# Kernel optimization log

Hardware: AMD Instinct MI355X
Metric: run time of the kernel (lower is better)

The kernel has to match this reference:

```python
import jax, jax.numpy as jnp
import numpy as np

N, D, C = 32768, 1024, 256
GAMMA = 1e-4


def setup_inputs() -> dict:
    key = jax.random.key(0)
    kx, kw = jax.random.split(key)
    X = jax.random.normal(kx, (N, D), dtype=jnp.float32)
    # lcls linear params: weight [C, D], bias [C] (torch nn.Linear layout)
    W = jax.random.normal(kw, (C, D), dtype=jnp.float32) * (1.0 / np.sqrt(D))
    b = jnp.zeros((C,), dtype=jnp.float32)
    return {"X": X, "W": W, "b": b}


def reference(X, W, b):
    # P = softmax(X @ W.T + b) over cluster dim C
    P = jax.nn.softmax(X @ W.T + b, axis=-1)            # [N, C]
    # Reorder P @ P.T @ X -> P @ (P.T @ X): avoids the O(N^2) affinity matrix
    PtX = jnp.einsum('nc,nd->cd', P, X)                  # [C, D]
    return X + GAMMA * (P @ PtX)                         # [N, D]
```

## Files before the change

kernel.cpp:

```cpp
#include <hip/hip_runtime.h>
#include <hip/hip_bf16.h>
#include <stdint.h>

#define N_TOK 32768
#define DIM   1024
#define NC    256
#define GAMMA_F 1e-4f

typedef unsigned short u16;
typedef __attribute__((ext_vector_type(8))) short bf16x8;
typedef __attribute__((ext_vector_type(4))) float f32x4;

__device__ __forceinline__ u16 f2b(float f) {
  union { float f; uint32_t u; } c; c.f = f;
  uint32_t u = c.u;
  return (u16)((u + 0x7FFFu + ((u >> 16) & 1u)) >> 16);
}

__device__ __forceinline__ void gll16(const void* g, void* l) {
  __builtin_amdgcn_global_load_lds(
      (const __attribute__((address_space(1))) unsigned int*)g,
      (__attribute__((address_space(3))) unsigned int*)l, 16, 0, 0);
}


__global__ __launch_bounds__(256) void k0_transpose(const float* __restrict__ X,
                                                    u16* __restrict__ TX) {
  __shared__ u16 tile[64][68];
  const int n0 = blockIdx.x * 64;
  const int d0 = blockIdx.y * 64;
  const int t = threadIdx.x;
  const int r = t >> 4;
  const int c4 = (t & 15) * 4;
#pragma unroll
  for (int i = 0; i < 4; ++i) {
    const int row = r + i * 16;
    const float4 v = *reinterpret_cast<const float4*>(&X[(size_t)(n0 + row) * DIM + d0 + c4]);
    tile[row][c4 + 0] = f2b(v.x);
    tile[row][c4 + 1] = f2b(v.y);
    tile[row][c4 + 2] = f2b(v.z);
    tile[row][c4 + 3] = f2b(v.w);
  }
  __syncthreads();
#pragma unroll
  for (int i = 0; i < 4; ++i) {
    const int drow = r + i * 16;
    ushort4 o;
    o.x = tile[c4 + 0][drow];
    o.y = tile[c4 + 1][drow];
    o.z = tile[c4 + 2][drow];
    o.w = tile[c4 + 3][drow];
    *reinterpret_cast<ushort4*>(&TX[(size_t)(d0 + drow) * N_TOK + n0 + c4]) = o;
  }
}

__global__ __launch_bounds__(256) void k0_convert_w(const float* __restrict__ W,
                                                    u16* __restrict__ Wb) {
  const int idx = (blockIdx.x * 256 + threadIdx.x) * 4;
  const float4 v = *reinterpret_cast<const float4*>(&W[idx]);
  ushort4 o;
  o.x = f2b(v.x); o.y = f2b(v.y); o.z = f2b(v.z); o.w = f2b(v.w);
  *reinterpret_cast<ushort4*>(&Wb[idx]) = o;
}

__global__ __launch_bounds__(256, 2) void p1_fused(const float* __restrict__ X,
                                                   const u16* __restrict__ Wb,
                                                   const float* __restrict__ bias,
                                                   u16* __restrict__ P,
                                                   u16* __restrict__ PT) {
  __shared__ __align__(16) char smem[66560];
  u16* As = (u16*)smem;
  u16* Bs = (u16*)(smem + 8192);
  const int t = threadIdx.x;
  const int lane = t & 63, wave = t >> 6;
  const int wm = wave & 1, wn = wave >> 1;
  const int n0 = blockIdx.x * 64;
  const int frow = lane & 15, fq = lane >> 4;
  const int au = t & 7, ar0 = t >> 3;
  const int bug = (lane & 7) ^ (lane >> 3);

  f32x4 acc[2][8] = {};
  for (int kt = 0; kt < 16; ++kt) {
    const int k0 = kt * 64;
#pragma unroll
    for (int h = 0; h < 2; ++h) {
      const int r = ar0 + h * 32;
      const size_t gb = (size_t)(n0 + r) * DIM + k0 + au * 8;
      const float4 v0 = *reinterpret_cast<const float4*>(&X[gb]);
      const float4 v1 = *reinterpret_cast<const float4*>(&X[gb + 4]);
      bf16x8 u;
      u[0] = (short)f2b(v0.x); u[1] = (short)f2b(v0.y);
      u[2] = (short)f2b(v0.z); u[3] = (short)f2b(v0.w);
      u[4] = (short)f2b(v1.x); u[5] = (short)f2b(v1.y);
      u[6] = (short)f2b(v1.z); u[7] = (short)f2b(v1.w);
      *reinterpret_cast<bf16x8*>(&As[r * 64 + ((au ^ (r & 7)) * 8)]) = u;
    }
#pragma unroll
    for (int i = 0; i < 8; ++i) {
      const int chunk = wave * 8 + i;
      const int brow = chunk * 8 + (lane >> 3);
      gll16(&Wb[(size_t)brow * DIM + k0 + bug * 8], &Bs[chunk * 512]);
    }
    __syncthreads();
#pragma unroll
    for (int ks = 0; ks < 2; ++ks) {
      bf16x8 af[2], bg[8];
#pragma unroll
      for (int m = 0; m < 2; ++m) {
        const int r = wm * 32 + m * 16 + frow;
        af[m] = *reinterpret_cast<const bf16x8*>(&As[r * 64 + (((ks * 4 + fq) ^ (r & 7)) * 8)]);
      }
#pragma unroll
      for (int n = 0; n < 8; ++n) {
        const int r = wn * 128 + n * 16 + frow;
        bg[n] = *reinterpret_cast<const bf16x8*>(&Bs[r * 64 + (((ks * 4 + fq) ^ (r & 7)) * 8)]);
      }
#pragma unroll
      for (int m = 0; m < 2; ++m)
#pragma unroll
        for (int n = 0; n < 8; ++n)
          acc[m][n] = __builtin_amdgcn_mfma_f32_16x16x32_bf16(af[m], bg[n], acc[m][n], 0, 0, 0);
    }
    __syncthreads();
  }
  float* Sf = (float*)smem;
#pragma unroll
  for (int m = 0; m < 2; ++m)
#pragma unroll
    for (int n = 0; n < 8; ++n) {
      const int row = wm * 32 + m * 16 + fq * 4;
      const int col = wn * 128 + n * 16 + frow;
#pragma unroll
      for (int j = 0; j < 4; ++j)
        Sf[(row + j) * 260 + col] = acc[m][n][j];
    }
  __syncthreads();
  u16* Su = (u16*)smem;
  const float4 bv = *reinterpret_cast<const float4*>(&bias[lane * 4]);
  const float l2e = 1.44269504088896f;
#pragma unroll
  for (int i = 0; i < 16; ++i) {
    const int row = wave * 16 + i;
    float4 v = *reinterpret_cast<const float4*>(&Sf[row * 260 + lane * 4]);
    v.x += bv.x; v.y += bv.y; v.z += bv.z; v.w += bv.w;
    float mx = fmaxf(fmaxf(v.x, v.y), fmaxf(v.z, v.w));
#pragma unroll
    for (int s = 1; s < 64; s <<= 1) mx = fmaxf(mx, __shfl_xor(mx, s, 64));
    const float e0 = exp2f((v.x - mx) * l2e), e1 = exp2f((v.y - mx) * l2e);
    const float e2 = exp2f((v.z - mx) * l2e), e3 = exp2f((v.w - mx) * l2e);
    float sm = e0 + e1 + e2 + e3;
#pragma unroll
    for (int s = 1; s < 64; s <<= 1) sm += __shfl_xor(sm, s, 64);
    const float inv = 1.0f / sm;
    ushort4 o;
    o.x = f2b(e0 * inv); o.y = f2b(e1 * inv);
    o.z = f2b(e2 * inv); o.w = f2b(e3 * inv);
    *reinterpret_cast<ushort4*>(&P[(size_t)(n0 + row) * NC + lane * 4]) = o;
    const int rb = row & 31;
    Su[row * 520 + (((lane * 4 + 0) ^ rb)) * 2] = o.x;
    Su[row * 520 + (((lane * 4 + 1) ^ rb)) * 2] = o.y;
    Su[row * 520 + (((lane * 4 + 2) ^ rb)) * 2] = o.z;
    Su[row * 520 + (((lane * 4 + 3) ^ rb)) * 2] = o.w;
  }
  __syncthreads();
#pragma unroll
  for (int it = 0; it < 16; ++it) {
    const int c = it * 16 + wave * 4 + fq;
    const int n = frow * 4;
    ushort4 o;
    o.x = Su[(n + 0) * 520 + ((c ^ ((n + 0) & 31))) * 2];
    o.y = Su[(n + 1) * 520 + ((c ^ ((n + 1) & 31))) * 2];
    o.z = Su[(n + 2) * 520 + ((c ^ ((n + 2) & 31))) * 2];
    o.w = Su[(n + 3) * 520 + ((c ^ ((n + 3) & 31))) * 2];
    *reinterpret_cast<ushort4*>(&PT[(size_t)c * N_TOK + n0 + n]) = o;
  }
}

__global__ __launch_bounds__(256, 2) void p2_gemm(const u16* __restrict__ TX,
                                                  const u16* __restrict__ PT,
                                                  float* __restrict__ part) {
  __shared__ __align__(16) char smem[67584];
  u16* As = (u16*)smem;
  u16* Bs = (u16*)(smem + 16384);
  const int t = threadIdx.x;
  const int lane = t & 63, wave = t >> 6;
  const int wm = wave & 1, wn = wave >> 1;
  const int sk = blockIdx.x;
  const int d0 = (blockIdx.y >> 1) * 128;
  const int c0 = (blockIdx.y & 1) * 128;
  const int frow = lane & 15, fq = lane >> 4;
  const int srow = lane >> 3;
  const int bug = (lane & 7) ^ (lane >> 3);
  f32x4 acc[4][4] = {};
  for (int kt = 0; kt < 16; ++kt) {
    const size_t k0 = (size_t)sk * 1024 + kt * 64;
#pragma unroll
    for (int i = 0; i < 4; ++i) {
      const int chunk = wave * 4 + i;
      const int r = chunk * 8 + srow;
      gll16(&TX[(size_t)(d0 + r) * N_TOK + k0 + bug * 8], &As[chunk * 512]);
      gll16(&PT[(size_t)(c0 + r) * N_TOK + k0 + bug * 8], &Bs[chunk * 512]);
    }
    __syncthreads();
#pragma unroll
    for (int ks = 0; ks < 2; ++ks) {
      bf16x8 af[4], bg[4];
#pragma unroll
      for (int m = 0; m < 4; ++m) {
        const int r = wm * 64 + m * 16 + frow;
        af[m] = *reinterpret_cast<const bf16x8*>(&As[r * 64 + (((ks * 4 + fq) ^ (r & 7)) * 8)]);
      }
#pragma unroll
      for (int n = 0; n < 4; ++n) {
        const int r = wn * 64 + n * 16 + frow;
        bg[n] = *reinterpret_cast<const bf16x8*>(&Bs[r * 64 + (((ks * 4 + fq) ^ (r & 7)) * 8)]);
      }
#pragma unroll
      for (int m = 0; m < 4; ++m)
#pragma unroll
        for (int n = 0; n < 4; ++n)
          acc[m][n] = __builtin_amdgcn_mfma_f32_16x16x32_bf16(af[m], bg[n], acc[m][n], 0, 0, 0);
    }
    __syncthreads();
  }
  float* Cf = (float*)smem;
#pragma unroll
  for (int m = 0; m < 4; ++m)
#pragma unroll
    for (int n = 0; n < 4; ++n) {
      const int row = wm * 64 + m * 16 + fq * 4;
      const int col = wn * 64 + n * 16 + frow;
#pragma unroll
      for (int j = 0; j < 4; ++j)
        Cf[(row + j) * 132 + col] = acc[m][n][j];
    }
  __syncthreads();
  float* pl = part + (size_t)sk * (DIM * NC);
  const int cl = (t & 31) * 4;
  const int rr = t >> 5;
#pragma unroll
  for (int p = 0; p < 16; ++p) {
    const int row = p * 8 + rr;
    const float4 v = *reinterpret_cast<const float4*>(&Cf[row * 132 + cl]);
    *reinterpret_cast<float4*>(&pl[(size_t)(d0 + row) * NC + c0 + cl]) = v;
  }
}

__global__ __launch_bounds__(256) void k2_reduce(const float* __restrict__ part,
                                                 u16* __restrict__ PtXb) {
  const int g = (blockIdx.x * 256 + threadIdx.x) * 4;
  f32x4 s = {0.f, 0.f, 0.f, 0.f};
#pragma unroll
  for (int p = 0; p < 32; ++p)
    s += *reinterpret_cast<const f32x4*>(&part[(size_t)p * (DIM * NC) + g]);
  ushort4 o;
  o.x = f2b(s[0] * GAMMA_F); o.y = f2b(s[1] * GAMMA_F);
  o.z = f2b(s[2] * GAMMA_F); o.w = f2b(s[3] * GAMMA_F);
  *reinterpret_cast<ushort4*>(&PtXb[g]) = o;
}

__global__ __launch_bounds__(256, 2) void p3_gemm(const u16* __restrict__ P,
                                                  const u16* __restrict__ PtXb,
                                                  const float* __restrict__ X,
                                                  float* __restrict__ Out) {
  __shared__ __align__(16) char smem[67584];
  u16* As = (u16*)smem;
  u16* Bs = (u16*)(smem + 16384);
  const int t = threadIdx.x;
  const int lane = t & 63, wave = t >> 6;
  const int wm = wave & 1, wn = wave >> 1;
  const int n0 = blockIdx.x * 128;
  const int d0 = blockIdx.y * 128;
  const int frow = lane & 15, fq = lane >> 4;
  const int srow = lane >> 3;
  const int bug = (lane & 7) ^ (lane >> 3);
  f32x4 acc[4][4] = {};
  for (int kt = 0; kt < 4; ++kt) {
    const int k0 = kt * 64;
#pragma unroll
    for (int i = 0; i < 4; ++i) {
      const int chunk = wave * 4 + i;
      const int r = chunk * 8 + srow;
      gll16(&P[(size_t)(n0 + r) * NC + k0 + bug * 8], &As[chunk * 512]);
      gll16(&PtXb[(size_t)(d0 + r) * NC + k0 + bug * 8], &Bs[chunk * 512]);
    }
    __syncthreads();
#pragma unroll
    for (int ks = 0; ks < 2; ++ks) {
      bf16x8 af[4], bg[4];
#pragma unroll
      for (int m = 0; m < 4; ++m) {
        const int r = wm * 64 + m * 16 + frow;
        af[m] = *reinterpret_cast<const bf16x8*>(&As[r * 64 + (((ks * 4 + fq) ^ (r & 7)) * 8)]);
      }
#pragma unroll
      for (int n = 0; n < 4; ++n) {
        const int r = wn * 64 + n * 16 + frow;
        bg[n] = *reinterpret_cast<const bf16x8*>(&Bs[r * 64 + (((ks * 4 + fq) ^ (r & 7)) * 8)]);
      }
#pragma unroll
      for (int m = 0; m < 4; ++m)
#pragma unroll
        for (int n = 0; n < 4; ++n)
          acc[m][n] = __builtin_amdgcn_mfma_f32_16x16x32_bf16(af[m], bg[n], acc[m][n], 0, 0, 0);
    }
    __syncthreads();
  }
  float* Cf = (float*)smem;
#pragma unroll
  for (int m = 0; m < 4; ++m)
#pragma unroll
    for (int n = 0; n < 4; ++n) {
      const int row = wm * 64 + m * 16 + fq * 4;
      const int col = wn * 64 + n * 16 + frow;
#pragma unroll
      for (int j = 0; j < 4; ++j)
        Cf[(row + j) * 132 + col] = acc[m][n][j];
    }
  __syncthreads();
  const int cl = (t & 31) * 4;
  const int rr = t >> 5;
#pragma unroll
  for (int p = 0; p < 16; ++p) {
    const int row = p * 8 + rr;
    float4 v = *reinterpret_cast<const float4*>(&Cf[row * 132 + cl]);
    const size_t off = (size_t)(n0 + row) * DIM + d0 + cl;
    const float4 x = *reinterpret_cast<const float4*>(&X[off]);
    v.x += x.x; v.y += x.y; v.z += x.z; v.w += x.w;
    *reinterpret_cast<float4*>(&Out[off]) = v;
  }
}

extern "C" void kernel_launch(void* const* d_in, const int* in_sizes, int n_in,
                              void* d_out, int out_size, void* d_ws, size_t ws_size,
                              hipStream_t stream) {
  const float* X = (const float*)d_in[0];
  const float* W = (const float*)d_in[1];
  const float* b = (const float*)d_in[2];
  float* Out = (float*)d_out;
  char* ws = (char*)d_ws;

  const size_t OFF_TX   = 0;
  const size_t OFF_WB   = (size_t)64 << 20;
  const size_t OFF_PTXB = OFF_WB + ((size_t)512 << 10);
  const size_t OFF_PART = (size_t)65 << 20;
  const size_t OFF_P    = (size_t)97 << 20;
  const size_t OFF_PT   = (size_t)113 << 20;
  const size_t NEED     = (size_t)129 << 20;
  if (ws_size < NEED) return;

  u16*   TX   = (u16*)(ws + OFF_TX);
  u16*   Wb   = (u16*)(ws + OFF_WB);
  u16*   PtXb = (u16*)(ws + OFF_PTXB);
  float* part = (float*)(ws + OFF_PART);
  u16*   Pp   = (u16*)(ws + OFF_P);
  u16*   PT   = (u16*)(ws + OFF_PT);

  k0_transpose<<<dim3(N_TOK / 64, DIM / 64), 256, 0, stream>>>(X, TX);
  k0_convert_w<<<dim3((NC * DIM) / 1024), 256, 0, stream>>>(W, Wb);
  p1_fused<<<dim3(N_TOK / 64), 256, 0, stream>>>(X, Wb, b, Pp, PT);
  p2_gemm<<<dim3(32, 16), 256, 0, stream>>>(TX, PT, part);
  k2_reduce<<<dim3((DIM * NC) / 1024), 256, 0, stream>>>(part, PtXb);
  p3_gemm<<<dim3(N_TOK / 128, DIM / 128), 256, 0, stream>>>(Pp, PtXb, X, Out);
}
```

Baseline: 378.4 us.

## Shrink LDS footprint for higher occupancy, softmax in registers, swizzle block order

The softmax in p1_fused now works directly on MFMA accumulators. It uses cross-lane shuffles plus a small LDS exchange for row max and sum, so the full fp32 score tile no longer goes through shared memory. The p2 and p3 epilogues stage output in two halves, which roughly halves LDS use. Together these let launch bounds rise to 4 blocks per CU. Block IDs are also remapped so consecutive blocks land on different tiles, which may help L2 or XCD locality. The cost is extra barriers in the epilogues and more register pressure, which could cause spills at 4 blocks per CU.

```diff
diff --git a/kernel.cpp b/kernel.cpp
--- a/kernel.cpp
+++ b/kernel.cpp
@@ -63,18 +63,19 @@
   *reinterpret_cast<ushort4*>(&Wb[idx]) = o;
 }
 
-__global__ __launch_bounds__(256, 2) void p1_fused(const float* __restrict__ X,
+__global__ __launch_bounds__(256, 4) void p1_fused(const float* __restrict__ X,
                                                    const u16* __restrict__ Wb,
                                                    const float* __restrict__ bias,
                                                    u16* __restrict__ P,
                                                    u16* __restrict__ PT) {
-  __shared__ __align__(16) char smem[66560];
+  __shared__ __align__(16) char smem[40960];
   u16* As = (u16*)smem;
   u16* Bs = (u16*)(smem + 8192);
   const int t = threadIdx.x;
   const int lane = t & 63, wave = t >> 6;
   const int wm = wave & 1, wn = wave >> 1;
-  const int n0 = blockIdx.x * 64;
+  const int id = blockIdx.x;
+  const int n0 = ((id & 7) * 64 + (id >> 3)) * 64;
   const int frow = lane & 15, fq = lane >> 4;
   const int au = t & 7, ar0 = t >> 3;
   const int bug = (lane & 7) ^ (lane >> 3);
@@ -123,71 +124,118 @@
     }
     __syncthreads();
   }
-  float* Sf = (float*)smem;
+
+  u16*   Su     = (u16*)smem;
+  float* red_mx = (float*)(smem + 33280);
+  float* red_sm = (float*)(smem + 33792);
+
+  float bias_r[8];
+#pragma unroll
+  for (int n = 0; n < 8; ++n) bias_r[n] = bias[wn * 128 + n * 16 + frow];
 #pragma unroll
   for (int m = 0; m < 2; ++m)
 #pragma unroll
-    for (int n = 0; n < 8; ++n) {
-      const int row = wm * 32 + m * 16 + fq * 4;
-      const int col = wn * 128 + n * 16 + frow;
+    for (int n = 0; n < 8; ++n)
+#pragma unroll
+      for (int j = 0; j < 4; ++j) acc[m][n][j] += bias_r[n];
+
+  float mx[2][4];
+#pragma unroll
+  for (int m = 0; m < 2; ++m)
+#pragma unroll
+    for (int j = 0; j < 4; ++j) {
+      float v = acc[m][0][j];
+#pragma unroll
+      for (int n = 1; n < 8; ++n) v = fmaxf(v, acc[m][n][j]);
+#pragma unroll
+      for (int s = 1; s < 16; s <<= 1) v = fmaxf(v, __shfl_xor(v, s, 64));
+      mx[m][j] = v;
+    }
+  if (frow == 0) {
+#pragma unroll
+    for (int m = 0; m < 2; ++m)
 #pragma unroll
       for (int j = 0; j < 4; ++j)
-        Sf[(row + j) * 260 + col] = acc[m][n][j];
-    }
+        red_mx[(wm * 32 + m * 16 + fq * 4 + j) * 2 + wn] = mx[m][j];
+  }
   __syncthreads();
-  u16* Su = (u16*)smem;
-  const float4 bv = *reinterpret_cast<const float4*>(&bias[lane * 4]);
+
   const float l2e = 1.44269504088896f;
-#pragma unroll
-  for (int i = 0; i < 16; ++i) {
-    const int row = wave * 16 + i;
-    float4 v = *reinterpret_cast<const float4*>(&Sf[row * 260 + lane * 4]);
-    v.x += bv.x; v.y += bv.y; v.z += bv.z; v.w += bv.w;
-    float mx = fmaxf(fmaxf(v.x, v.y), fmaxf(v.z, v.w));
-#pragma unroll
-    for (int s = 1; s < 64; s <<= 1) mx = fmaxf(mx, __shfl_xor(mx, s, 64));
-    const float e0 = exp2f((v.x - mx) * l2e), e1 = exp2f((v.y - mx) * l2e);
-    const float e2 = exp2f((v.z - mx) * l2e), e3 = exp2f((v.w - mx) * l2e);
-    float sm = e0 + e1 + e2 + e3;
-#pragma unroll
-    for (int s = 1; s < 64; s <<= 1) sm += __shfl_xor(sm, s, 64);
-    const float inv = 1.0f / sm;
-    ushort4 o;
-    o.x = f2b(e0 * inv); o.y = f2b(e1 * inv);
-    o.z = f2b(e2 * inv); o.w = f2b(e3 * inv);
-    *reinterpret_cast<ushort4*>(&P[(size_t)(n0 + row) * NC + lane * 4]) = o;
-    const int rb = row & 31;
-    Su[row * 520 + (((lane * 4 + 0) ^ rb)) * 2] = o.x;
-    Su[row * 520 + (((lane * 4 + 1) ^ rb)) * 2] = o.y;
-    Su[row * 520 + (((lane * 4 + 2) ^ rb)) * 2] = o.z;
-    Su[row * 520 + (((lane * 4 + 3) ^ rb)) * 2] = o.w;
+  float psum[2][4];
+#pragma unroll
+  for (int m = 0; m < 2; ++m)
+#pragma unroll
+    for (int j = 0; j < 4; ++j) {
+      const int row = wm * 32 + m * 16 + fq * 4 + j;
+      const float2 r2 = *reinterpret_cast<const float2*>(&red_mx[row * 2]);
+      const float M = fmaxf(r2.x, r2.y);
+      float s = 0.f;
+#pragma unroll
+      for (int n = 0; n < 8; ++n) {
+        const float e = exp2f((acc[m][n][j] - M) * l2e);
+        acc[m][n][j] = e;
+        s += e;
+      }
+#pragma unroll
+      for (int ss = 1; ss < 16; ss <<= 1) s += __shfl_xor(s, ss, 64);
+      psum[m][j] = s;
+    }
+  if (frow == 0) {
+#pragma unroll
+    for (int m = 0; m < 2; ++m)
+#pragma unroll
+      for (int j = 0; j < 4; ++j)
+        red_sm[(wm * 32 + m * 16 + fq * 4 + j) * 2 + wn] = psum[m][j];
   }
   __syncthreads();
+
+#pragma unroll
+  for (int m = 0; m < 2; ++m)
+#pragma unroll
+    for (int j = 0; j < 4; ++j) {
+      const int row = wm * 32 + m * 16 + fq * 4 + j;
+      const float2 r2 = *reinterpret_cast<const float2*>(&red_sm[row * 2]);
+      const float iv = 1.0f / (r2.x + r2.y);
+#pragma unroll
+      for (int n = 0; n < 8; ++n)
+        Su[row * 260 + wn * 128 + n * 16 + frow] = f2b(acc[m][n][j] * iv);
+    }
+  __syncthreads();
+
+#pragma unroll
+  for (int g = 0; g < 16; ++g) {
+    const int row = g * 4 + wave;
+    const int c = lane * 4;
+    const ushort4 v = *reinterpret_cast<const ushort4*>(&Su[row * 260 + c]);
+    *reinterpret_cast<ushort4*>(&P[(size_t)(n0 + row) * NC + c]) = v;
+  }
 #pragma unroll
   for (int it = 0; it < 16; ++it) {
     const int c = it * 16 + wave * 4 + fq;
     const int n = frow * 4;
     ushort4 o;
-    o.x = Su[(n + 0) * 520 + ((c ^ ((n + 0) & 31))) * 2];
-    o.y = Su[(n + 1) * 520 + ((c ^ ((n + 1) & 31))) * 2];
-    o.z = Su[(n + 2) * 520 + ((c ^ ((n + 2) & 31))) * 2];
-    o.w = Su[(n + 3) * 520 + ((c ^ ((n + 3) & 31))) * 2];
+    o.x = Su[(n + 0) * 260 + c];
+    o.y = Su[(n + 1) * 260 + c];
+    o.z = Su[(n + 2) * 260 + c];
+    o.w = Su[(n + 3) * 260 + c];
     *reinterpret_cast<ushort4*>(&PT[(size_t)c * N_TOK + n0 + n]) = o;
   }
 }
 
-__global__ __launch_bounds__(256, 2) void p2_gemm(const u16* __restrict__ TX,
+__global__ __launch_bounds__(256, 4) void p2_gemm(const u16* __restrict__ TX,
                                                   const u16* __restrict__ PT,
                                                   float* __restrict__ part) {
-  __shared__ __align__(16) char smem[67584];
+  __shared__ __align__(16) char smem[34816];
   u16* As = (u16*)smem;
   u16* Bs = (u16*)(smem + 16384);
   const int t = threadIdx.x;
   const int lane = t & 63, wave = t >> 6;
   const int wm = wave & 1, wn = wave >> 1;
-  const int sk = blockIdx.x;
-  const int d0 = (blockIdx.y >> 1) * 128;
-  const int c0 = (blockIdx.y & 1) * 128;
+  const int id = blockIdx.x;
+  const int swz = (id & 7) * 64 + (id >> 3);
+  const int d0 = (swz & 7) * 128;
+  const int sk = (swz >> 3) & 31;
+  const int c0 = (swz >> 8) * 128;
   const int frow = lane & 15, fq = lane >> 4;
   const int srow = lane >> 3;
   const int bug = (lane & 7) ^ (lane >> 3);
@@ -224,25 +272,31 @@
     __syncthreads();
   }
   float* Cf = (float*)smem;
-#pragma unroll
-  for (int m = 0; m < 4; ++m)
-#pragma unroll
-    for (int n = 0; n < 4; ++n) {
-      const int row = wm * 64 + m * 16 + fq * 4;
-      const int col = wn * 64 + n * 16 + frow;
-#pragma unroll
-      for (int j = 0; j < 4; ++j)
-        Cf[(row + j) * 132 + col] = acc[m][n][j];
-    }
-  __syncthreads();
   float* pl = part + (size_t)sk * (DIM * NC);
   const int cl = (t & 31) * 4;
-  const int rr = t >> 5;
-#pragma unroll
-  for (int p = 0; p < 16; ++p) {
-    const int row = p * 8 + rr;
-    const float4 v = *reinterpret_cast<const float4*>(&Cf[row * 132 + cl]);
-    *reinterpret_cast<float4*>(&pl[(size_t)(d0 + row) * NC + c0 + cl]) = v;
+  const int rq = t >> 5;
+#pragma unroll
+  for (int h = 0; h < 2; ++h) {
+    __syncthreads();
+    if (wm == h) {
+#pragma unroll
+      for (int m = 0; m < 4; ++m)
+#pragma unroll
+        for (int n = 0; n < 4; ++n) {
+          const int rr = m * 16 + fq * 4;
+          const int col = wn * 64 + n * 16 + frow;
+#pragma unroll
+          for (int j = 0; j < 4; ++j)
+            Cf[(rr + j) * 132 + col] = acc[m][n][j];
+        }
+    }
+    __syncthreads();
+#pragma unroll
+    for (int p = 0; p < 8; ++p) {
+      const int row = p * 8 + rq;
+      const float4 v = *reinterpret_cast<const float4*>(&Cf[row * 132 + cl]);
+      *reinterpret_cast<float4*>(&pl[(size_t)(d0 + h * 64 + row) * NC + c0 + cl]) = v;
+    }
   }
 }
 
@@ -259,18 +313,20 @@
   *reinterpret_cast<ushort4*>(&PtXb[g]) = o;
 }
 
-__global__ __launch_bounds__(256, 2) void p3_gemm(const u16* __restrict__ P,
+__global__ __launch_bounds__(256, 4) void p3_gemm(const u16* __restrict__ P,
                                                   const u16* __restrict__ PtXb,
                                                   const float* __restrict__ X,
                                                   float* __restrict__ Out) {
-  __shared__ __align__(16) char smem[67584];
+  __shared__ __align__(16) char smem[34816];
   u16* As = (u16*)smem;
   u16* Bs = (u16*)(smem + 16384);
   const int t = threadIdx.x;
   const int lane = t & 63, wave = t >> 6;
   const int wm = wave & 1, wn = wave >> 1;
-  const int n0 = blockIdx.x * 128;
-  const int d0 = blockIdx.y * 128;
+  const int id = blockIdx.x;
+  const int swz = (id & 7) * 256 + (id >> 3);
+  const int n0 = (swz & 255) * 128;
+  const int d0 = (swz >> 8) * 128;
   const int frow = lane & 15, fq = lane >> 4;
   const int srow = lane >> 3;
   const int bug = (lane & 7) ^ (lane >> 3);
@@ -307,27 +363,33 @@
     __syncthreads();
   }
   float* Cf = (float*)smem;
-#pragma unroll
-  for (int m = 0; m < 4; ++m)
-#pragma unroll
-    for (int n = 0; n < 4; ++n) {
-      const int row = wm * 64 + m * 16 + fq * 4;
-      const int col = wn * 64 + n * 16 + frow;
-#pragma unroll
-      for (int j = 0; j < 4; ++j)
-        Cf[(row + j) * 132 + col] = acc[m][n][j];
-    }
-  __syncthreads();
   const int cl = (t & 31) * 4;
-  const int rr = t >> 5;
-#pragma unroll
-  for (int p = 0; p < 16; ++p) {
-    const int row = p * 8 + rr;
-    float4 v = *reinterpret_cast<const float4*>(&Cf[row * 132 + cl]);
-    const size_t off = (size_t)(n0 + row) * DIM + d0 + cl;
-    const float4 x = *reinterpret_cast<const float4*>(&X[off]);
-    v.x += x.x; v.y += x.y; v.z += x.z; v.w += x.w;
-    *reinterpret_cast<float4*>(&Out[off]) = v;
+  const int rq = t >> 5;
+#pragma unroll
+  for (int h = 0; h < 2; ++h) {
+    __syncthreads();
+    if (wm == h) {
+#pragma unroll
+      for (int m = 0; m < 4; ++m)
+#pragma unroll
+        for (int n = 0; n < 4; ++n) {
+          const int rr = m * 16 + fq * 4;
+          const int col = wn * 64 + n * 16 + frow;
+#pragma unroll
+          for (int j = 0; j < 4; ++j)
+            Cf[(rr + j) * 132 + col] = acc[m][n][j];
+        }
+    }
+    __syncthreads();
+#pragma unroll
+    for (int p = 0; p < 8; ++p) {
+      const int row = p * 8 + rq;
+      float4 v = *reinterpret_cast<const float4*>(&Cf[row * 132 + cl]);
+      const size_t off = (size_t)(n0 + h * 64 + row) * DIM + d0 + cl;
+      const float4 x = *reinterpret_cast<const float4*>(&X[off]);
+      v.x += x.x; v.y += x.y; v.z += x.z; v.w += x.w;
+      *reinterpret_cast<float4*>(&Out[off]) = v;
+    }
   }
 }
 
@@ -359,7 +421,7 @@
   k0_transpose<<<dim3(N_TOK / 64, DIM / 64), 256, 0, stream>>>(X, TX);
   k0_convert_w<<<dim3((NC * DIM) / 1024), 256, 0, stream>>>(W, Wb);
   p1_fused<<<dim3(N_TOK / 64), 256, 0, stream>>>(X, Wb, b, Pp, PT);
-  p2_gemm<<<dim3(32, 16), 256, 0, stream>>>(TX, PT, part);
+  p2_gemm<<<dim3(512), 256, 0, stream>>>(TX, PT, part);
   k2_reduce<<<dim3((DIM * NC) / 1024), 256, 0, stream>>>(part, PtXb);
-  p3_gemm<<<dim3(N_TOK / 128, DIM / 128), 256, 0, stream>>>(Pp, PtXb, X, Out);
-}
+  p3_gemm<<<dim3(2048), 256, 0, stream>>>(Pp, PtXb, X, Out);
+}
```

After: 405.7 us. 1.07x slower.
